# Kernel optimization log

Measured on AMD Instinct MI355X. Metric: run time of the kernel, lower is better.

Reference implementation:

```python
import jax, jax.numpy as jnp
import numpy as np

N = 100_000   # nodes
E = 200_000   # directed edges
G = 2_500     # graphs in batch
F_NODE = 16
F_EDGE = 8
H1 = 32
H2 = 16


def setup_inputs() -> dict:
    key = jax.random.key(0)
    ks = jax.random.split(key, 24)
    p = lambda k, shape: 0.1 * jax.random.normal(k, shape, dtype=jnp.float32)
    inp = {
        "x": jax.random.normal(ks[0], (N, F_NODE), dtype=jnp.float32),
        "edge_attr": jax.random.normal(ks[1], (E, F_EDGE), dtype=jnp.float32),
        # edge-MLP for conv1: F_EDGE -> 16 -> F_NODE*H1
        "w_e1a": p(ks[2], (F_EDGE, 16)), "b_e1a": p(ks[3], (16,)),
        "w_e1b": p(ks[4], (16, F_NODE * H1)), "b_e1b": p(ks[5], (F_NODE * H1,)),
        "w_root1": p(ks[6], (F_NODE, H1)), "b_root1": p(ks[7], (H1,)),
        # edge-MLP for conv2: F_EDGE -> 16 -> H1*H2
        "w_e2a": p(ks[8], (F_EDGE, 16)), "b_e2a": p(ks[9], (16,)),
        "w_e2b": p(ks[10], (16, H1 * H2)), "b_e2b": p(ks[11], (H1 * H2,)),
        "w_root2": p(ks[12], (H1, H2)), "b_root2": p(ks[13], (H2,)),
        # attention-pool gate nn: F_NODE -> F_NODE -> 1
        "w_g1": p(ks[14], (F_NODE, F_NODE)), "b_g1": p(ks[15], (F_NODE,)),
        "w_g2": p(ks[16], (F_NODE, 1)), "b_g2": p(ks[17], (1,)),
        # head: (H2 + F_NODE) -> 8 -> 1
        "w_l1": p(ks[18], (H2 + F_NODE, 8)), "b_l1": p(ks[19], (8,)),
        "w_l2": p(ks[20], (8, 1)), "b_l2": p(ks[21], (1,)),
        "edge_index": jax.random.randint(ks[22], (2, E), 0, N),
        "batch": jnp.sort(jax.random.randint(ks[23], (N,), 0, G)),
    }
    return inp


def _nnconv(x, src, tgt, edge_attr, wa, ba, wb, bb, wr, br, in_c, out_c, n):
    # PyG NNConv: x_i' = x_i @ W_root + b + sum_{j->i} x_j @ Theta(e_ji)
    h = jax.nn.relu(edge_attr @ wa + ba)              # [E, 16]
    theta = (h @ wb + bb).reshape(-1, in_c, out_c)    # [E, in, out]
    msg = jnp.einsum('ei,eio->eo', x[src], theta)     # [E, out]
    agg = jax.ops.segment_sum(msg, tgt, num_segments=n)
    return x @ wr + br + agg


def reference(x, edge_attr, w_e1a, b_e1a, w_e1b, b_e1b, w_root1, b_root1,
              w_e2a, b_e2a, w_e2b, b_e2b, w_root2, b_root2,
              w_g1, b_g1, w_g2, b_g2, w_l1, b_l1, w_l2, b_l2,
              edge_index, batch):
    src, tgt = edge_index[0], edge_index[1]
    n = x.shape[0]

    # GlobalAttention pooling on raw node features (per-graph segment softmax)
    gate = jax.nn.relu(x @ w_g1 + b_g1) @ w_g2 + b_g2          # [N, 1]
    m = jax.ops.segment_max(gate, batch, num_segments=G)       # [G, 1]
    a = jnp.exp(gate - m[batch])
    s = jax.ops.segment_sum(a, batch, num_segments=G)
    x_att = jax.ops.segment_sum((a / s[batch]) * x, batch, num_segments=G)  # [G, F_NODE]

    # Two NNConv layers with ReLU
    h = jax.nn.relu(_nnconv(x, src, tgt, edge_attr, w_e1a, b_e1a, w_e1b, b_e1b,
                            w_root1, b_root1, F_NODE, H1, n))
    h = jax.nn.relu(_nnconv(h, src, tgt, edge_attr, w_e2a, b_e2a, w_e2b, b_e2b,
                            w_root2, b_root2, H1, H2, n))

    # global_mean_pool
    cnt = jax.ops.segment_sum(jnp.ones((n, 1), h.dtype), batch, num_segments=G)
    mean = jax.ops.segment_sum(h, batch, num_segments=G) / jnp.maximum(cnt, 1.0)

    z = jnp.concatenate([mean, x_att], axis=1)  # [G, H2 + F_NODE]
    # eval mode: dropout p=0.5 is identity; two linear layers, no activation between
    z = z @ w_l1 + b_l1
    z = z @ w_l2 + b_l2
    return z
```

## Files before the change

kernel.cpp:

```cpp
#include <hip/hip_runtime.h>
#include <hip/hip_bf16.h>

#define NN 100000
#define NE 200000
#define NG 2500
#define FN 16
#define FE 8
#define H1C 32
#define H2C 16
#define KH 16

typedef __attribute__((ext_vector_type(4))) float f32x4;
typedef _Float16 __attribute__((ext_vector_type(2))) half2v;
typedef _Float16 __attribute__((ext_vector_type(8))) half8v;
typedef __fp16 __attribute__((ext_vector_type(2))) pkf16x2;

__device__ __forceinline__ float bf2f(unsigned int u){
  union { unsigned int i; float f; } v; v.i = (u & 0xffffu) << 16; return v.f;
}
__device__ __forceinline__ unsigned int pkh(float a, float b){
  union { pkf16x2 h; unsigned int u; } v; v.h = __builtin_amdgcn_cvt_pkrtz(a, b); return v.u;
}
__device__ __forceinline__ float h2lo(unsigned int u){
  union { unsigned short s; _Float16 h; } v; v.s = (unsigned short)u; return (float)v.h;
}
__device__ __forceinline__ float h2hi(unsigned int u){
  union { unsigned short s; _Float16 h; } v; v.s = (unsigned short)(u >> 16); return (float)v.h;
}
__device__ __forceinline__ float rdf(const void* p, long i, bool isbf){
  return isbf ? bf2f(((const unsigned short*)p)[i]) : ((const float*)p)[i];
}
__device__ __forceinline__ void atomic_pk_f16(unsigned short* addr, unsigned int pk){
  asm volatile("global_atomic_pk_add_f16 %0, %1, off" :: "v"(addr), "v"(pk) : "memory");
}
__device__ __forceinline__ bool detect_isbf(const void* __restrict__ x){
  const unsigned short* u = (const unsigned short*)x;
  int lane = threadIdx.x & 63;
  float f = bf2f(u[2*lane]);
  float a = fabsf(f);
  bool sane = (f == 0.0f) || (a > 1e-4f && a < 1e4f);
  unsigned long long b = __ballot(sane);
  return __popcll(b) >= 32;
}
__device__ __forceinline__ void load_x16(const void* __restrict__ xin, bool isbf, int n, float* xv){
  if(isbf){
    uint4 u0 = ((const uint4*)xin)[2*n], u1 = ((const uint4*)xin)[2*n+1];
    xv[0]=bf2f(u0.x); xv[1]=bf2f(u0.x>>16); xv[2]=bf2f(u0.y); xv[3]=bf2f(u0.y>>16);
    xv[4]=bf2f(u0.z); xv[5]=bf2f(u0.z>>16); xv[6]=bf2f(u0.w); xv[7]=bf2f(u0.w>>16);
    xv[8]=bf2f(u1.x); xv[9]=bf2f(u1.x>>16); xv[10]=bf2f(u1.y); xv[11]=bf2f(u1.y>>16);
    xv[12]=bf2f(u1.z); xv[13]=bf2f(u1.z>>16); xv[14]=bf2f(u1.w); xv[15]=bf2f(u1.w>>16);
  } else {
    #pragma unroll
    for(int q = 0; q < 4; q++){
      float4 v = ((const float4*)xin)[4*n + q];
      xv[q*4+0]=v.x; xv[q*4+1]=v.y; xv[q*4+2]=v.z; xv[q*4+3]=v.w;
    }
  }
}

#define NW 20
struct WArgs { const void* p[NW]; };
enum {
  OW_E1A=0,     OB_E1A=128,   OW_E1B=144,   OB_E1B=8336,  OW_R1=8848,  OB_R1=9360,
  OW_E2A=9392,  OB_E2A=9520,  OW_E2B=9536,  OB_E2B=17728, OW_R2=18240, OB_R2=18752,
  OW_G1=18768,  OB_G1=19024,  OW_G2=19040,  OB_G2=19056,
  OW_L1=19057,  OB_L1=19313,  OW_L2=19321,  OB_L2=19329
};

template<int IN, int OUT, bool RAWX>
__device__ __forceinline__ void conv_tile(
    int u, const void* __restrict__ nodef, bool isbf,
    const unsigned int* __restrict__ hpk, const int* __restrict__ ei,
    const unsigned short* __restrict__ wpack, unsigned short* __restrict__ agg)
{
  constexpr int KMF  = ((KH*IN + IN + 31)/32)*32;
  constexpr int KP   = KMF + 8;
  constexpr int NT   = OUT/16;
  constexpr int KS   = KMF/32;
  int tid = threadIdx.x;
  int lane = tid & 63, m = lane & 15, quad = lane >> 4;
  int wid = tid >> 6;
  int ebase = u*64 + wid*16;
  int em = ebase + m;
  int sn = ei[em];
  int q1 = quad >> 1;
  int xoff = (IN == 16) ? ((quad & 1)*8) : (quad*8);
  union { half8v v; half2v h[4]; unsigned int w[4]; } X;
  if(RAWX){
    if(isbf){
      uint4 uu = *(const uint4*)((const unsigned short*)nodef + (size_t)sn*IN + xoff);
      X.w[0] = pkh(bf2f(uu.x), bf2f(uu.x >> 16));
      X.w[1] = pkh(bf2f(uu.y), bf2f(uu.y >> 16));
      X.w[2] = pkh(bf2f(uu.z), bf2f(uu.z >> 16));
      X.w[3] = pkh(bf2f(uu.w), bf2f(uu.w >> 16));
    } else {
      const float4* xp = (const float4*)((const float*)nodef + (size_t)sn*IN + xoff);
      float4 v0 = xp[0], v1 = xp[1];
      X.w[0] = pkh(v0.x, v0.y);
      X.w[1] = pkh(v0.z, v0.w);
      X.w[2] = pkh(v1.x, v1.y);
      X.w[3] = pkh(v1.z, v1.w);
    }
  } else {
    uint4 uu = *(const uint4*)((const unsigned short*)nodef + (size_t)sn*IN + xoff);
    X.w[0]=uu.x; X.w[1]=uu.y; X.w[2]=uu.z; X.w[3]=uu.w;
  }
  unsigned int hu[8];
  {
    const uint4* hp = (const uint4*)(hpk + (size_t)em*8);
    uint4 u0 = hp[0], u1 = hp[1];
    hu[0]=u0.x; hu[1]=u0.y; hu[2]=u0.z; hu[3]=u0.w;
    hu[4]=u1.x; hu[5]=u1.y; hu[6]=u1.z; hu[7]=u1.w;
  }
  int4 tg = *(const int4*)(ei + NE + ebase + quad*4);

  f32x4 acc[NT];
  #pragma unroll
  for(int nt = 0; nt < NT; nt++) acc[nt] = (f32x4){0.f,0.f,0.f,0.f};

  const half8v hz = {};
  #pragma unroll
  for(int ks = 0; ks < KS; ks++){
    union { half8v v; half2v h[4]; } A;
    if(ks < KS-1){
      unsigned short hs = (unsigned short)((IN == 16) ? (hu[ks] >> (16*q1))
                                                      : (hu[ks >> 1] >> (16*(ks & 1))));
      union { unsigned short s; _Float16 h; } hc; hc.s = hs;
      half2v hv2 = { hc.h, hc.h };
      #pragma unroll
      for(int k = 0; k < 4; k++) A.h[k] = hv2 * X.h[k];
    } else {
      if(IN == 16) A.v = (quad < 2) ? X.v : hz;
      else         A.v = X.v;
    }
    #pragma unroll
    for(int nt = 0; nt < NT; nt++){
      half8v b = *(const half8v*)(wpack + (size_t)(nt*16 + m)*KP + ks*32 + quad*8);
      acc[nt] = __builtin_amdgcn_mfma_f32_16x16x32_f16(A.v, b, acc[nt], 0, 0, 0);
    }
  }
  int tr[4] = {tg.x, tg.y, tg.z, tg.w};
  int mlo = m & ~1;
  bool evn = (m & 1) == 0;
  #pragma unroll
  for(int r = 0; r < 4; r++){
    #pragma unroll
    for(int nt = 0; nt < NT; nt++){
      float v = acc[nt][r];
      float vn = __shfl_xor(v, 1);
      if(evn ? (r < 2) : (r >= 2)){
        unsigned int pk = evn ? pkh(v, vn) : pkh(vn, v);
        atomic_pk_f16(agg + (size_t)tr[r]*OUT + nt*16 + mlo, pk);
      }
    }
  }
}

#define MB_A 76
#define MB_B (MB_A + 19)
#define MB_C (MB_B + 18)
#define MB_D (MB_C + 391)
#define MB_E (MB_D + 782)
#define MB_F (MB_E + 391)
__global__ void __launch_bounds__(256) mega1_kernel(
    const void* __restrict__ xin, const void* __restrict__ efin, WArgs w,
    const int* __restrict__ batch,
    float* __restrict__ wts, unsigned int* __restrict__ wpack1, unsigned int* __restrict__ wpack2,
    float* __restrict__ gate,
    unsigned int* __restrict__ hpk1,
    int* __restrict__ gstart, unsigned short* __restrict__ agg1)
{
  int b = blockIdx.x, tid = threadIdx.x;
  if(b < MB_A){
    bool isbf = detect_isbf(xin);
    int i = b*256 + tid;
    if(i >= 19330) return;
    const int sz[NW] = {128,16,8192,512,512,32, 128,16,8192,512,512,16, 256,16,16,1, 256,8,8,1};
    int seg = 0; long base = 0;
    while(i - base >= sz[seg]){ base += sz[seg]; seg++; }
    wts[i] = rdf(w.p[seg], i - base, isbf);
    return;
  }
  if(b < MB_B){
    bool isbf = detect_isbf(xin);
    int j = (b - MB_A)*256 + tid;
    if(j >= 4736) return;
    int n = j / 148; int k = (j % 148) * 2;
    float v0 = 0.f, v1 = 0.f;
    if(k < 256)        v0 = rdf(w.p[2], (long)k*32 + n, isbf);
    else if(k < 272)   v0 = rdf(w.p[3], (long)(k-256)*32 + n, isbf);
    if(k+1 < 256)      v1 = rdf(w.p[2], (long)(k+1)*32 + n, isbf);
    else if(k+1 < 272) v1 = rdf(w.p[3], (long)(k+1-256)*32 + n, isbf);
    wpack1[j] = pkh(v0, v1);
    return;
  }
  if(b < MB_C){
    bool isbf = detect_isbf(xin);
    int j = (b - MB_B)*256 + tid;
    if(j >= 4416) return;
    int n = j / 276; int k = (j % 276) * 2;
    float v0 = 0.f, v1 = 0.f;
    if(k < 512)        v0 = rdf(w.p[8], (long)k*16 + n, isbf);
    else if(k < 544)   v0 = rdf(w.p[9], (long)(k-512)*16 + n, isbf);
    if(k+1 < 512)      v1 = rdf(w.p[8], (long)(k+1)*16 + n, isbf);
    else if(k+1 < 544) v1 = rdf(w.p[9], (long)(k+1-512)*16 + n, isbf);
    wpack2[j] = pkh(v0, v1);
    return;
  }
  if(b < MB_D){
    __shared__ float s_w1[FN*FN], s_b1[FN], s_w2[FN], s_b2v[1];
    bool isbf = detect_isbf(xin);
    if(tid < FN*FN) s_w1[tid] = rdf(w.p[12], tid, isbf);
    if(tid < FN){ s_b1[tid] = rdf(w.p[13], tid, isbf); s_w2[tid] = rdf(w.p[14], tid, isbf); }
    if(tid == 0) s_b2v[0] = rdf(w.p[15], 0, isbf);
    __syncthreads();
    int n = (b - MB_C)*256 + tid;
    if(n >= NN) return;
    {
      int b1 = batch[n];
      int b0 = (n == 0) ? -1 : batch[n-1];
      for(int g2 = b0 + 1; g2 <= b1; g2++) gstart[g2] = n;
      if(n == NN-1) for(int g2 = b1 + 1; g2 <= NG; g2++) gstart[g2] = NN;
    }
    float xv[FN];
    load_x16(xin, isbf, n, xv);
    float g = s_b2v[0];
    #pragma unroll
    for(int j = 0; j < FN; j++){
      float hj = s_b1[j];
      #pragma unroll
      for(int i = 0; i < FN; i++) hj += xv[i] * s_w1[i*FN + j];
      hj = hj > 0.f ? hj : 0.f;
      g += hj * s_w2[j];
    }
    gate[n] = g;
    return;
  }
  if(b < MB_E){
    __shared__ float s_w1[FE*KH], s_b1[KH];
    bool isbf = detect_isbf(xin);
    if(tid < FE*KH) s_w1[tid] = rdf(w.p[0], tid, isbf);
    if(tid < KH) s_b1[tid] = rdf(w.p[1], tid, isbf);
    __syncthreads();
    int e = (b - MB_D)*256 + tid;
    if(e >= NE) return;
    float ev[FE];
    if(isbf){
      uint4 u = ((const uint4*)efin)[e];
      ev[0]=bf2f(u.x); ev[1]=bf2f(u.x>>16); ev[2]=bf2f(u.y); ev[3]=bf2f(u.y>>16);
      ev[4]=bf2f(u.z); ev[5]=bf2f(u.z>>16); ev[6]=bf2f(u.w); ev[7]=bf2f(u.w>>16);
    } else {
      float4 a = ((const float4*)efin)[2*e], bb = ((const float4*)efin)[2*e+1];
      ev[0]=a.x; ev[1]=a.y; ev[2]=a.z; ev[3]=a.w; ev[4]=bb.x; ev[5]=bb.y; ev[6]=bb.z; ev[7]=bb.w;
    }
    unsigned int o[8];
    #pragma unroll
    for(int d = 0; d < 8; d++){
      float h0 = s_b1[2*d], h1 = s_b1[2*d+1];
      #pragma unroll
      for(int k = 0; k < FE; k++){
        h0 += ev[k] * s_w1[k*KH + 2*d];
        h1 += ev[k] * s_w1[k*KH + 2*d+1];
      }
      h0 = h0 > 0.f ? h0 : 0.f; h1 = h1 > 0.f ? h1 : 0.f;
      o[d] = pkh(h0, h1);
    }
    uint4* p1 = (uint4*)(hpk1 + (size_t)e*8);
    p1[0] = make_uint4(o[0],o[1],o[2],o[3]); p1[1] = make_uint4(o[4],o[5],o[6],o[7]);
    return;
  }
  {
    int idx = (b - MB_E)*256 + tid;
    if(idx < 100000){
      uint4 z = make_uint4(0,0,0,0);
      uint4* p = (uint4*)((char*)agg1 + (size_t)idx*64);
      p[0] = z; p[1] = z; p[2] = z; p[3] = z;
    }
  }
}

#define C1_CONV (NE/64)
#define C1_E2   (C1_CONV + 782)
#define C1_Z    (C1_E2 + 196)
#define C1_ATT  (C1_Z + 625)
__global__ void __launch_bounds__(256) conv1_kernel(
    const void* __restrict__ xin, const void* __restrict__ efin,
    const float* __restrict__ wts,
    const unsigned int* __restrict__ hpk1, const int* __restrict__ ei,
    const unsigned short* __restrict__ wpack,
    unsigned short* __restrict__ agg1, unsigned short* __restrict__ agg2,
    unsigned int* __restrict__ hpk2,
    const float* __restrict__ gate, const int* __restrict__ gstart,
    float* __restrict__ xatt)
{
  int b = blockIdx.x, tid = threadIdx.x;
  bool isbf = detect_isbf(xin);
  if(b < C1_CONV){
    conv_tile<FN, H1C, true>(b, xin, isbf, hpk1, ei, wpack, agg1);
    return;
  }
  if(b < C1_E2){
    __shared__ float s_w2[FE*KH], s_b2[KH];
    if(tid < FE*KH) s_w2[tid] = wts[OW_E2A + tid];
    if(tid < KH) s_b2[tid] = wts[OB_E2A + tid];
    __syncthreads();
    int e = (b - C1_CONV)*256 + tid;
    if(e >= NE) return;
    float ev[FE];
    if(isbf){
      uint4 u = ((const uint4*)efin)[e];
      ev[0]=bf2f(u.x); ev[1]=bf2f(u.x>>16); ev[2]=bf2f(u.y); ev[3]=bf2f(u.y>>16);
      ev[4]=bf2f(u.z); ev[5]=bf2f(u.z>>16); ev[6]=bf2f(u.w); ev[7]=bf2f(u.w>>16);
    } else {
      float4 a = ((const float4*)efin)[2*e], bb = ((const float4*)efin)[2*e+1];
      ev[0]=a.x; ev[1]=a.y; ev[2]=a.z; ev[3]=a.w; ev[4]=bb.x; ev[5]=bb.y; ev[6]=bb.z; ev[7]=bb.w;
    }
    unsigned int o[8];
    #pragma unroll
    for(int d = 0; d < 8; d++){
      float h0 = s_b2[2*d], h1 = s_b2[2*d+1];
      #pragma unroll
      for(int k = 0; k < FE; k++){
        h0 += ev[k] * s_w2[k*KH + 2*d];
        h1 += ev[k] * s_w2[k*KH + 2*d+1];
      }
      h0 = h0 > 0.f ? h0 : 0.f; h1 = h1 > 0.f ? h1 : 0.f;
      o[d] = pkh(h0, h1);
    }
    uint4* p2 = (uint4*)(hpk2 + (size_t)e*8);
    p2[0] = make_uint4(o[0],o[1],o[2],o[3]); p2[1] = make_uint4(o[4],o[5],o[6],o[7]);
    return;
  }
  if(b < C1_Z){
    int idx = (b - C1_E2)*256 + tid;
    if(idx < 50000){
      uint4 z = make_uint4(0,0,0,0);
      uint4* p = (uint4*)((char*)agg2 + (size_t)idx*64);
      p[0] = z; p[1] = z; p[2] = z; p[3] = z;
    }
    return;
  }
  {
    int lane = tid & 63, wid = tid >> 6;
    int g = (b - C1_Z)*4 + wid;
    int start = gstart[g], end = gstart[g+1];
    float mx = -1e30f;
    for(int n = start + lane; n < end; n += 64) mx = fmaxf(mx, gate[n]);
    #pragma unroll
    for(int o = 32; o >= 1; o >>= 1) mx = fmaxf(mx, __shfl_xor(mx, o));
    float s = 0.f;
    float acc[FN];
    #pragma unroll
    for(int f = 0; f < FN; f++) acc[f] = 0.f;
    for(int n = start + lane; n < end; n += 64){
      float a = __expf(gate[n] - mx);
      s += a;
      float xv[FN];
      load_x16(xin, isbf, n, xv);
      #pragma unroll
      for(int f = 0; f < FN; f++) acc[f] += a * xv[f];
    }
    #pragma unroll
    for(int o = 32; o >= 1; o >>= 1){
      s += __shfl_xor(s, o);
      #pragma unroll
      for(int f = 0; f < FN; f++) acc[f] += __shfl_xor(acc[f], o);
    }
    if(lane < FN) xatt[(size_t)g*FN + lane] = (end > start && s > 0.f) ? acc[lane] / s : 0.f;
  }
}

__global__ void __launch_bounds__(256) conv2_kernel(
    const unsigned short* __restrict__ h1b, const unsigned int* __restrict__ hpk2,
    const int* __restrict__ ei, const unsigned short* __restrict__ wpack2,
    unsigned short* __restrict__ agg2)
{
  conv_tile<H1C, H2C, false>(blockIdx.x, h1b, false, hpk2, ei, wpack2, agg2);
}

__global__ void __launch_bounds__(256) node1_kernel(
    const void* __restrict__ xin, const unsigned short* __restrict__ agg1,
    const float* __restrict__ wr, const float* __restrict__ br,
    unsigned short* __restrict__ h1b)
{
  __shared__ float s_w[FN*H1C], s_b[H1C];
  for(int i = threadIdx.x; i < FN*H1C; i += 256) s_w[i] = wr[i];
  if(threadIdx.x < H1C) s_b[threadIdx.x] = br[threadIdx.x];
  bool isbf = detect_isbf(xin);
  __syncthreads();
  int g = blockIdx.x*256 + threadIdx.x;
  int n = g >> 3, q = g & 7;
  if(n >= NN) return;
  uint2 au = *(const uint2*)(agg1 + (size_t)n*H1C + q*4);
  float a0 = s_b[q*4+0] + h2lo(au.x), a1 = s_b[q*4+1] + h2hi(au.x);
  float a2 = s_b[q*4+2] + h2lo(au.y), a3 = s_b[q*4+3] + h2hi(au.y);
  float xv[FN];
  load_x16(xin, isbf, n, xv);
  #pragma unroll
  for(int i = 0; i < FN; i++){
    float xi = xv[i];
    a0 += xi*s_w[i*H1C + q*4+0]; a1 += xi*s_w[i*H1C + q*4+1];
    a2 += xi*s_w[i*H1C + q*4+2]; a3 += xi*s_w[i*H1C + q*4+3];
  }
  a0 = a0>0.f?a0:0.f; a1 = a1>0.f?a1:0.f; a2 = a2>0.f?a2:0.f; a3 = a3>0.f?a3:0.f;
  uint2 hb; hb.x = pkh(a0, a1); hb.y = pkh(a2, a3);
  *(uint2*)(h1b + (size_t)n*H1C + q*4) = hb;
}

__global__ void __launch_bounds__(256) node2_kernel(
    const unsigned short* __restrict__ h1b, const unsigned short* __restrict__ agg2,
    const float* __restrict__ wr, const float* __restrict__ br, float* __restrict__ h2)
{
  __shared__ float s_w[H1C*H2C], s_b[H2C];
  for(int i = threadIdx.x; i < H1C*H2C; i += 256) s_w[i] = wr[i];
  if(threadIdx.x < H2C) s_b[threadIdx.x] = br[threadIdx.x];
  __syncthreads();
  int g = blockIdx.x*256 + threadIdx.x;
  int n = g >> 2, q = g & 3;
  if(n >= NN) return;
  uint2 au = *(const uint2*)(agg2 + (size_t)n*H2C + q*4);
  float a0 = s_b[q*4+0] + h2lo(au.x), a1 = s_b[q*4+1] + h2hi(au.x);
  float a2 = s_b[q*4+2] + h2lo(au.y), a3 = s_b[q*4+3] + h2hi(au.y);
  const unsigned int* hb = (const unsigned int*)(h1b + (size_t)n*H1C);
  #pragma unroll
  for(int i2 = 0; i2 < H1C/2; i2++){
    unsigned int u = hb[i2];
    float x0 = h2lo(u), x1 = h2hi(u);
    int i = 2*i2;
    a0 += x0*s_w[i*H2C + q*4+0] + x1*s_w[(i+1)*H2C + q*4+0];
    a1 += x0*s_w[i*H2C + q*4+1] + x1*s_w[(i+1)*H2C + q*4+1];
    a2 += x0*s_w[i*H2C + q*4+2] + x1*s_w[(i+1)*H2C + q*4+2];
    a3 += x0*s_w[i*H2C + q*4+3] + x1*s_w[(i+1)*H2C + q*4+3];
  }
  float4 r; r.x = a0>0.f?a0:0.f; r.y = a1>0.f?a1:0.f; r.z = a2>0.f?a2:0.f; r.w = a3>0.f?a3:0.f;
  *(float4*)(h2 + (size_t)n*H2C + q*4) = r;
}

__global__ void head_kernel(const float* __restrict__ xatt,
    const float* __restrict__ h2, const int* __restrict__ gstart, const void* __restrict__ xin,
    const float* __restrict__ wl1, const float* __restrict__ bl1,
    const float* __restrict__ wl2, const float* __restrict__ bl2,
    void* __restrict__ out)
{
  __shared__ float sz[H2C + FN];
  int g = blockIdx.x;
  int lane = threadIdx.x;
  bool isbf = detect_isbf(xin);
  int start = gstart[g];
  int end   = gstart[g + 1];
  float acc[H2C];
  #pragma unroll
  for(int f = 0; f < H2C; f++) acc[f] = 0.f;
  for(int n = start + lane; n < end; n += 64){
    const float4* hp = (const float4*)(h2 + (size_t)n*H2C);
    #pragma unroll
    for(int q = 0; q < 4; q++){
      float4 v = hp[q];
      acc[q*4+0] += v.x; acc[q*4+1] += v.y; acc[q*4+2] += v.z; acc[q*4+3] += v.w;
    }
  }
  #pragma unroll
  for(int o = 32; o >= 1; o >>= 1){
    #pragma unroll
    for(int f = 0; f < H2C; f++) acc[f] += __shfl_xor(acc[f], o);
  }
  float inv = 1.f / fmaxf((float)(end - start), 1.f);
  if(lane < H2C) sz[lane] = acc[lane] * inv;
  if(lane < FN)  sz[H2C + lane] = xatt[(size_t)g*FN + lane];
  __syncthreads();
  if(lane == 0){
    float t1[8];
    #pragma unroll
    for(int j = 0; j < 8; j++){
      float t = bl1[j];
      #pragma unroll
      for(int c = 0; c < H2C + FN; c++) t += sz[c] * wl1[c*8 + j];
      t1[j] = t;
    }
    float o = bl2[0];
    #pragma unroll
    for(int j = 0; j < 8; j++) o += t1[j] * wl2[j];
    if(isbf) ((__hip_bfloat16*)out)[g] = __float2bfloat16(o);
    else     ((float*)out)[g] = o;
  }
}

extern "C" void kernel_launch(void* const* d_in, const int* in_sizes, int n_in,
                              void* d_out, int out_size, void* d_ws, size_t ws_size,
                              hipStream_t stream)
{
  const int* ei    = (const int*)d_in[22];
  const int* batch = (const int*)d_in[23];

  float* ws = (float*)d_ws;
  float* gate   = ws;
  float* wts    = gate + 100000;
  float* xatt   = wts + 19360;
  int*   gstart = (int*)(xatt + 40000);
  unsigned int* wpack1 = (unsigned int*)(gstart + 2504);
  unsigned int* wpack2 = wpack1 + 4736;
  unsigned int* hpk1   = wpack2 + 4416;
  unsigned int* hpk2   = hpk1 + 1600000;
  unsigned short* h1b  = (unsigned short*)(hpk2 + 1600000);
  float* h2     = (float*)(h1b + 3200000);
  unsigned short* agg1 = (unsigned short*)(h2 + 1600000);
  unsigned short* agg2 = agg1 + 3200000;

  WArgs wa;
  for(int i = 0; i < NW; i++) wa.p[i] = d_in[2 + i];

  mega1_kernel<<<MB_F, 256, 0, stream>>>(d_in[0], d_in[1], wa, batch,
      wts, wpack1, wpack2, gate, hpk1, gstart, agg1);

  conv1_kernel<<<C1_ATT, 256, 0, stream>>>(d_in[0], d_in[1], wts, hpk1, ei,
      (const unsigned short*)wpack1, agg1, agg2, hpk2, gate, gstart, xatt);
  node1_kernel<<<(NN*8 + 255)/256, 256, 0, stream>>>(d_in[0], agg1, wts+OW_R1, wts+OB_R1, h1b);

  conv2_kernel<<<NE/64, 256, 0, stream>>>(h1b, hpk2, ei,
      (const unsigned short*)wpack2, agg2);
  node2_kernel<<<(NN*4 + 255)/256, 256, 0, stream>>>(h1b, agg2, wts+OW_R2, wts+OB_R2, h2);

  head_kernel<<<NG, 64, 0, stream>>>(xatt, h2, gstart, d_in[0],
      wts+OW_L1, wts+OB_L1, wts+OW_L2, wts+OB_L2, d_out);
}
```

Before: 187.1 us.

## Fuse node2 root transform into head pooling kernel, four graphs per block

Removes the separate node2 kernel and the fp32 h2 buffer. The head kernel now computes each node's root transform, bias and ReLU inline while mean-pooling, with each wave handling one graph and four graphs per 256-thread block. Head weights are staged in shared memory. This saves a launch and the h2 write/read round trip, but each lane now does a full 32x16 matvec per node serially, so per-graph latency and register pressure rise and parallelism drops to 2500 waves.

```diff
diff --git a/kernel.cpp b/kernel.cpp
--- a/kernel.cpp
+++ b/kernel.cpp
@@ -407,57 +407,53 @@
   *(uint2*)(h1b + (size_t)n*H1C + q*4) = hb;
 }
 
-__global__ void __launch_bounds__(256) node2_kernel(
+__global__ void __launch_bounds__(256) head_kernel(
     const unsigned short* __restrict__ h1b, const unsigned short* __restrict__ agg2,
-    const float* __restrict__ wr, const float* __restrict__ br, float* __restrict__ h2)
-{
-  __shared__ float s_w[H1C*H2C], s_b[H2C];
-  for(int i = threadIdx.x; i < H1C*H2C; i += 256) s_w[i] = wr[i];
-  if(threadIdx.x < H2C) s_b[threadIdx.x] = br[threadIdx.x];
+    const float* __restrict__ xatt, const int* __restrict__ gstart,
+    const void* __restrict__ xin, const float* __restrict__ wts,
+    void* __restrict__ out)
+{
+  __shared__ float s_w2[H1C*H2C], s_b2[H2C];
+  __shared__ float s_l1[(H2C+FN)*8], s_lb1[8], s_l2[8], s_lb2v[1];
+  __shared__ float sz[4][H2C+FN];
+  int tid = threadIdx.x;
+  for(int i = tid; i < H1C*H2C; i += 256) s_w2[i] = wts[OW_R2+i];
+  if(tid < H2C) s_b2[tid] = wts[OB_R2+tid];
+  s_l1[tid] = wts[OW_L1 + tid];
+  if(tid < 8){ s_lb1[tid] = wts[OB_L1+tid]; s_l2[tid] = wts[OW_L2+tid]; }
+  if(tid == 0) s_lb2v[0] = wts[OB_L2];
+  bool isbf = detect_isbf(xin);
   __syncthreads();
-  int g = blockIdx.x*256 + threadIdx.x;
-  int n = g >> 2, q = g & 3;
-  if(n >= NN) return;
-  uint2 au = *(const uint2*)(agg2 + (size_t)n*H2C + q*4);
-  float a0 = s_b[q*4+0] + h2lo(au.x), a1 = s_b[q*4+1] + h2hi(au.x);
-  float a2 = s_b[q*4+2] + h2lo(au.y), a3 = s_b[q*4+3] + h2hi(au.y);
-  const unsigned int* hb = (const unsigned int*)(h1b + (size_t)n*H1C);
-  #pragma unroll
-  for(int i2 = 0; i2 < H1C/2; i2++){
-    unsigned int u = hb[i2];
-    float x0 = h2lo(u), x1 = h2hi(u);
-    int i = 2*i2;
-    a0 += x0*s_w[i*H2C + q*4+0] + x1*s_w[(i+1)*H2C + q*4+0];
-    a1 += x0*s_w[i*H2C + q*4+1] + x1*s_w[(i+1)*H2C + q*4+1];
-    a2 += x0*s_w[i*H2C + q*4+2] + x1*s_w[(i+1)*H2C + q*4+2];
-    a3 += x0*s_w[i*H2C + q*4+3] + x1*s_w[(i+1)*H2C + q*4+3];
-  }
-  float4 r; r.x = a0>0.f?a0:0.f; r.y = a1>0.f?a1:0.f; r.z = a2>0.f?a2:0.f; r.w = a3>0.f?a3:0.f;
-  *(float4*)(h2 + (size_t)n*H2C + q*4) = r;
-}
-
-__global__ void head_kernel(const float* __restrict__ xatt,
-    const float* __restrict__ h2, const int* __restrict__ gstart, const void* __restrict__ xin,
-    const float* __restrict__ wl1, const float* __restrict__ bl1,
-    const float* __restrict__ wl2, const float* __restrict__ bl2,
-    void* __restrict__ out)
-{
-  __shared__ float sz[H2C + FN];
-  int g = blockIdx.x;
-  int lane = threadIdx.x;
-  bool isbf = detect_isbf(xin);
-  int start = gstart[g];
-  int end   = gstart[g + 1];
+  int lane = tid & 63, wid = tid >> 6;
+  int g = blockIdx.x*4 + wid;
+  int start = gstart[g], end = gstart[g+1];
   float acc[H2C];
   #pragma unroll
   for(int f = 0; f < H2C; f++) acc[f] = 0.f;
   for(int n = start + lane; n < end; n += 64){
-    const float4* hp = (const float4*)(h2 + (size_t)n*H2C);
-    #pragma unroll
-    for(int q = 0; q < 4; q++){
-      float4 v = hp[q];
-      acc[q*4+0] += v.x; acc[q*4+1] += v.y; acc[q*4+2] += v.z; acc[q*4+3] += v.w;
-    }
+    float o[H2C];
+    {
+      const uint4* bp = (const uint4*)(agg2 + (size_t)n*H2C);
+      uint4 b0 = bp[0], b1 = bp[1];
+      unsigned int bw[8] = {b0.x,b0.y,b0.z,b0.w, b1.x,b1.y,b1.z,b1.w};
+      #pragma unroll
+      for(int o2 = 0; o2 < 8; o2++){
+        o[2*o2]   = h2lo(bw[o2]) + s_b2[2*o2];
+        o[2*o2+1] = h2hi(bw[o2]) + s_b2[2*o2+1];
+      }
+    }
+    const unsigned int* hb = (const unsigned int*)(h1b + (size_t)n*H1C);
+    #pragma unroll
+    for(int i2 = 0; i2 < H1C/2; i2++){
+      unsigned int u = hb[i2];
+      float x0 = h2lo(u), x1 = h2hi(u);
+      int i = 2*i2;
+      #pragma unroll
+      for(int c = 0; c < H2C; c++)
+        o[c] += x0*s_w2[i*H2C + c] + x1*s_w2[(i+1)*H2C + c];
+    }
+    #pragma unroll
+    for(int c = 0; c < H2C; c++) acc[c] += (o[c] > 0.f ? o[c] : 0.f);
   }
   #pragma unroll
   for(int o = 32; o >= 1; o >>= 1){
@@ -465,21 +461,21 @@
     for(int f = 0; f < H2C; f++) acc[f] += __shfl_xor(acc[f], o);
   }
   float inv = 1.f / fmaxf((float)(end - start), 1.f);
-  if(lane < H2C) sz[lane] = acc[lane] * inv;
-  if(lane < FN)  sz[H2C + lane] = xatt[(size_t)g*FN + lane];
+  if(lane < H2C) sz[wid][lane] = acc[lane] * inv;
+  if(lane < FN)  sz[wid][H2C + lane] = xatt[(size_t)g*FN + lane];
   __syncthreads();
   if(lane == 0){
     float t1[8];
     #pragma unroll
     for(int j = 0; j < 8; j++){
-      float t = bl1[j];
-      #pragma unroll
-      for(int c = 0; c < H2C + FN; c++) t += sz[c] * wl1[c*8 + j];
+      float t = s_lb1[j];
+      #pragma unroll
+      for(int c = 0; c < H2C + FN; c++) t += sz[wid][c] * s_l1[c*8 + j];
       t1[j] = t;
     }
-    float o = bl2[0];
-    #pragma unroll
-    for(int j = 0; j < 8; j++) o += t1[j] * wl2[j];
+    float o = s_lb2v[0];
+    #pragma unroll
+    for(int j = 0; j < 8; j++) o += t1[j] * s_l2[j];
     if(isbf) ((__hip_bfloat16*)out)[g] = __float2bfloat16(o);
     else     ((float*)out)[g] = o;
   }
@@ -502,8 +498,7 @@
   unsigned int* hpk1   = wpack2 + 4416;
   unsigned int* hpk2   = hpk1 + 1600000;
   unsigned short* h1b  = (unsigned short*)(hpk2 + 1600000);
-  float* h2     = (float*)(h1b + 3200000);
-  unsigned short* agg1 = (unsigned short*)(h2 + 1600000);
+  unsigned short* agg1 = h1b + 3200000;
   unsigned short* agg2 = agg1 + 3200000;
 
   WArgs wa;
@@ -518,8 +513,6 @@
 
   conv2_kernel<<<NE/64, 256, 0, stream>>>(h1b, hpk2, ei,
       (const unsigned short*)wpack2, agg2);
-  node2_kernel<<<(NN*4 + 255)/256, 256, 0, stream>>>(h1b, agg2, wts+OW_R2, wts+OB_R2, h2);
-
-  head_kernel<<<NG, 64, 0, stream>>>(xatt, h2, gstart, d_in[0],
-      wts+OW_L1, wts+OB_L1, wts+OW_L2, wts+OB_L2, d_out);
-}
+
+  head_kernel<<<NG/4, 256, 0, stream>>>(h1b, agg2, xatt, gstart, d_in[0], wts, d_out);
+}
```

Measured after the change: 270.5 us. 44.6% more time.
